# Kernel tuning notes

Measured on AMD Instinct MI355X. Metric: run time of the kernel, lower is better.

Reference implementation:

```python
import jax, jax.numpy as jnp
import numpy as np

B, S, D = 16, 1024, 768
H = 12
HD = D // H  # 64


def setup_inputs() -> dict:
    key = jax.random.key(0)
    k1, k2, k3 = jax.random.split(key, 3)
    scale_in = 1.0 / np.sqrt(D)
    return {
        "x": jax.random.normal(k1, (B, S, D), dtype=jnp.float32),
        "w_qkv": jax.random.normal(k2, (3 * D, D), dtype=jnp.float32) * scale_in,
        "b_qkv": jnp.zeros((3 * D,), dtype=jnp.float32),
        "w_proj": jax.random.normal(k3, (D, D), dtype=jnp.float32) * scale_in,
        "b_proj": jnp.zeros((D,), dtype=jnp.float32),
    }


def reference(x, w_qkv, b_qkv, w_proj, b_proj):
    b, s, d = x.shape
    scale = HD ** -0.5
    # qkv projection: [B,S,3D] -> [3,B,H,S,HD]
    qkv = x @ w_qkv.T + b_qkv
    qkv = qkv.reshape(b, s, 3, H, HD).transpose(2, 0, 3, 1, 4)
    q, k, v = qkv[0], qkv[1], qkv[2]
    q = q * scale
    attn = jnp.einsum("bhqd,bhkd->bhqk", q, k)  # [B,H,S,S]
    attn = jax.nn.softmax(attn, axis=-1)
    # attn_dropout is identity in eval mode
    z = jnp.einsum("bhqk,bhkd->bhqd", attn, v)
    z = z.transpose(0, 2, 1, 3).reshape(b, s, d)
    return z @ w_proj.T + b_proj
```

## Files before the change

### kernel.cpp

```cpp
#include <hip/hip_runtime.h>
#include <hip/hip_bf16.h>
#include <cstdint>
#include <cstddef>

typedef __attribute__((ext_vector_type(8))) short short8;
typedef __attribute__((ext_vector_type(4))) float floatx4;
typedef __attribute__((ext_vector_type(16))) float floatx16;
typedef unsigned short u16;

__device__ __forceinline__ u16 f2bf(float f) {
  unsigned u = __float_as_uint(f);
  u += 0x7FFFu + ((u >> 16) & 1u);
  return (u16)(u >> 16);
}

__device__ __forceinline__ unsigned cvt_pk_bf16(float a, float b) {
  unsigned r;
  asm("v_cvt_pk_bf16_f32 %0, %1, %2" : "=v"(r) : "v"(a), "v"(b));
  return r;
}

__device__ __forceinline__ float fexp2(float x) {
#if __has_builtin(__builtin_amdgcn_exp2f)
  return __builtin_amdgcn_exp2f(x);
#else
  float r;
  asm("v_exp_f32 %0, %1\n\ts_nop 1" : "=v"(r) : "v"(x));
  return r;
#endif
}

__device__ __forceinline__ float frcp(float x) {
#if __has_builtin(__builtin_amdgcn_rcpf)
  return __builtin_amdgcn_rcpf(x);
#else
  float r;
  asm("v_rcp_f32 %0, %1\n\ts_nop 1" : "=v"(r) : "v"(x));
  return r;
#endif
}

__device__ __forceinline__ void gload16(const u16* g, u16* l) {
  __builtin_amdgcn_global_load_lds(
      (const __attribute__((address_space(1))) void*)g,
      (__attribute__((address_space(3))) void*)l, 16, 0, 0);
}

__device__ __forceinline__ void phase_barrier() {
  __builtin_amdgcn_sched_barrier(0);
  __builtin_amdgcn_s_barrier();
  __builtin_amdgcn_sched_barrier(0);
}

#define MFMA16(a, b, c) __builtin_amdgcn_mfma_f32_16x16x32_bf16((a), (b), (c), 0, 0, 0)

__global__ void cvt3_kernel(const float* __restrict__ a, u16* __restrict__ oa, int na4,
                            const float* __restrict__ b, u16* __restrict__ ob, int nb4,
                            const float* __restrict__ c, u16* __restrict__ oc, int nc4) {
  int i = blockIdx.x * blockDim.x + threadIdx.x;
  int stride = gridDim.x * blockDim.x;
  int ntot = na4 + nb4 + nc4;
  for (int idx = i; idx < ntot; idx += stride) {
    const float* src; u16* dst; int j = idx;
    if (j < na4)            { src = a; dst = oa; }
    else if (j < na4 + nb4) { src = b; dst = ob; j -= na4; }
    else                    { src = c; dst = oc; j -= na4 + nb4; }
    float4 v = reinterpret_cast<const float4*>(src)[j];
    ushort4 o = make_ushort4(f2bf(v.x), f2bf(v.y), f2bf(v.z), f2bf(v.w));
    reinterpret_cast<ushort4*>(dst)[j] = o;
  }
}

template<bool OUTF32>
__global__ __launch_bounds__(512) void gemm_bt256_8p(
    const u16* __restrict__ A, const u16* __restrict__ B,
    const float* __restrict__ bias, void* __restrict__ Cout,
    int M, int N, int K, int qcols, float qscale)
{
  __shared__ u16 As[4 * 8192];
  __shared__ u16 Bs[4 * 8192];
  const int tid = threadIdx.x;
  const int lane = tid & 63, w = tid >> 6;
  const int l15 = lane & 15, lhi = lane >> 4;
  const int wm = w >> 2, wn = w & 3;

  const int mblocks = M >> 8;
  const int nb = N >> 8;
  const int bid = blockIdx.x;
  const int xcd = bid & 7;
  const int local = bid >> 3;
  const int mpx = mblocks >> 3;
  const int m0 = (xcd * mpx + local / nb) << 8;
  const int n0 = (local % nb) << 8;

  const int trow = tid >> 3;
  const int cg8 = ((tid & 7) ^ ((tid >> 4) & 7)) * 8;
  const u16* aS = A + (size_t)(m0 + trow) * K + cg8;
  const u16* bS = B + (size_t)(n0 + trow) * K + cg8;
  const int ksteps = K >> 6;

  const int x7 = (l15 >> 1) & 7;
  const int ko0 = l15 * 64 + (lhi ^ x7) * 8;
  const int ko1 = l15 * 64 + ((4 + lhi) ^ x7) * 8;
  const int brow = (wn & 1) * 64;

  floatx4 acc[8][4] = {};

#define STG(matS, lds, v, h) do { \
    gload16((matS) + (size_t)((h) * 128) * K + (size_t)(v) * 64, \
            (lds) + ((((v) & 1) * 2 + (h)) * 8192) + w * 512); \
    gload16((matS) + (size_t)((h) * 128 + 64) * K + (size_t)(v) * 64, \
            (lds) + ((((v) & 1) * 2 + (h)) * 8192) + 4096 + w * 512); \
  } while (0)

  STG(aS, As, 0, 0); STG(aS, As, 0, 1);
  STG(bS, Bs, 0, 0); STG(bS, Bs, 0, 1);
  if (ksteps > 1) {
    STG(bS, Bs, 1, 0); STG(bS, Bs, 1, 1);
    asm volatile("s_waitcnt vmcnt(4)" ::: "memory");
  } else {
    asm volatile("s_waitcnt vmcnt(0)" ::: "memory");
  }
  phase_barrier();

  for (int u = 0; u < ksteps; ++u) {
    const int so = (u & 1) * 16384;
    const u16* Ab = As + so + wm * 8192;
    const u16* Bb = Bs + so + (wn >> 1) * 8192;
    short8 af[4][2], bf[4][2];

#pragma unroll
    for (int i = 0; i < 4; ++i) {
      af[i][0] = *reinterpret_cast<const short8*>(Ab + (i * 16) * 64 + ko0);
      af[i][1] = *reinterpret_cast<const short8*>(Ab + (i * 16) * 64 + ko1);
    }
#pragma unroll
    for (int j = 0; j < 2; ++j) {
      bf[j][0] = *reinterpret_cast<const short8*>(Bb + (brow + j * 16) * 64 + ko0);
      bf[j][1] = *reinterpret_cast<const short8*>(Bb + (brow + j * 16) * 64 + ko1);
    }
    if (u + 1 < ksteps) STG(aS, As, u + 1, 0);
    phase_barrier();
    __builtin_amdgcn_s_setprio(1);
#pragma unroll
    for (int i = 0; i < 4; ++i)
#pragma unroll
      for (int j = 0; j < 2; ++j) {
        acc[i][j] = MFMA16(af[i][0], bf[j][0], acc[i][j]);
        acc[i][j] = MFMA16(af[i][1], bf[j][1], acc[i][j]);
      }
    __builtin_amdgcn_s_setprio(0);
    phase_barrier();

#pragma unroll
    for (int j = 2; j < 4; ++j) {
      bf[j][0] = *reinterpret_cast<const short8*>(Bb + (brow + 32 + (j - 2) * 16) * 64 + ko0);
      bf[j][1] = *reinterpret_cast<const short8*>(Bb + (brow + 32 + (j - 2) * 16) * 64 + ko1);
    }
    if (u + 1 < ksteps) STG(aS, As, u + 1, 1);
    phase_barrier();
    __builtin_amdgcn_s_setprio(1);
#pragma unroll
    for (int i = 0; i < 4; ++i)
#pragma unroll
      for (int j = 2; j < 4; ++j) {
        acc[i][j] = MFMA16(af[i][0], bf[j][0], acc[i][j]);
        acc[i][j] = MFMA16(af[i][1], bf[j][1], acc[i][j]);
      }
    __builtin_amdgcn_s_setprio(0);
    phase_barrier();

#pragma unroll
    for (int i = 0; i < 4; ++i) {
      af[i][0] = *reinterpret_cast<const short8*>(Ab + (64 + i * 16) * 64 + ko0);
      af[i][1] = *reinterpret_cast<const short8*>(Ab + (64 + i * 16) * 64 + ko1);
    }
    if (u + 2 < ksteps) STG(bS, Bs, u + 2, 0);
    phase_barrier();
    __builtin_amdgcn_s_setprio(1);
#pragma unroll
    for (int i = 0; i < 4; ++i)
#pragma unroll
      for (int j = 0; j < 2; ++j) {
        acc[4 + i][j] = MFMA16(af[i][0], bf[j][0], acc[4 + i][j]);
        acc[4 + i][j] = MFMA16(af[i][1], bf[j][1], acc[4 + i][j]);
      }
    __builtin_amdgcn_s_setprio(0);
    phase_barrier();

    if (u + 2 < ksteps) STG(bS, Bs, u + 2, 1);
    phase_barrier();
    __builtin_amdgcn_s_setprio(1);
#pragma unroll
    for (int i = 0; i < 4; ++i)
#pragma unroll
      for (int j = 2; j < 4; ++j) {
        acc[4 + i][j] = MFMA16(af[i][0], bf[j][0], acc[4 + i][j]);
        acc[4 + i][j] = MFMA16(af[i][1], bf[j][1], acc[4 + i][j]);
      }
    __builtin_amdgcn_s_setprio(0);
    if (u + 1 < ksteps) {
      if (u + 2 < ksteps) asm volatile("s_waitcnt vmcnt(4)" ::: "memory");
      else                asm volatile("s_waitcnt vmcnt(0)" ::: "memory");
    }
    phase_barrier();
  }
#undef STG

#pragma unroll
  for (int i = 0; i < 8; ++i)
#pragma unroll
    for (int j = 0; j < 4; ++j) {
      int row = m0 + wm * 128 + i * 16 + lhi * 4;
      int col = n0 + wn * 64 + j * 16 + l15;
      float bv = bias[col];
      float sc = (col < qcols) ? qscale : 1.0f;
#pragma unroll
      for (int r = 0; r < 4; ++r) {
        float v = (acc[i][j][r] + bv) * sc;
        if (OUTF32) reinterpret_cast<float*>(Cout)[(size_t)(row + r) * N + col] = v;
        else        reinterpret_cast<u16*>(Cout)[(size_t)(row + r) * N + col] = f2bf(v);
      }
    }
}

__global__ __launch_bounds__(256) void vtrans_kernel(
    const u16* __restrict__ qkv, u16* __restrict__ vt)
{
  __shared__ u16 T[64][72];
  const int idx = blockIdx.x;
  const int st = idx & 15;
  const int bh = idx >> 4;
  const int b = bh / 12, h = bh % 12;
  const int t = threadIdx.x;
  const int r2 = t >> 3, c8 = (t & 7) * 8;

  const u16* src = qkv + ((size_t)(b * 1024 + st * 64)) * 2304 + 1536 + h * 64;
#pragma unroll
  for (int rr = 0; rr < 2; ++rr) {
    int s = rr * 32 + r2;
    short8 v = *reinterpret_cast<const short8*>(src + (size_t)s * 2304 + c8);
    *reinterpret_cast<short8*>(&T[s][c8]) = v;
  }
  __syncthreads();
  u16* dst = vt + (size_t)bh * 64 * 1024 + st * 64;
#pragma unroll
  for (int rr = 0; rr < 2; ++rr) {
    int d = rr * 32 + r2;
    short8 o;
#pragma unroll
    for (int j = 0; j < 8; ++j) o[j] = T[c8 + j][d];
    *reinterpret_cast<short8*>(dst + (size_t)d * 1024 + c8) = o;
  }
}

__global__ __launch_bounds__(512) void attn9_kernel(
    const u16* __restrict__ qkv, const u16* __restrict__ vt, u16* __restrict__ z)
{
  constexpr int LDK = 72;
  constexpr int SLOT = 64 * LDK;
  __shared__ u16 Ks[2 * SLOT];
  __shared__ u16 Vs[2 * SLOT];

  const int tid = threadIdx.x;
  const int lane = tid & 63, w = tid >> 6;
  const int l31 = lane & 31, hi = lane >> 5;

  const int idx = blockIdx.x;
  const int head = idx % 192;
  const int qt   = idx / 192;
  const int b = head / 12, h = head % 12;

  const size_t rowbase = (size_t)b * 1024;
  const u16* Qp  = qkv + rowbase * 2304 + h * 64;
  const u16* Kp  = Qp + 768;
  const u16* Vtp = vt + (size_t)head * 64 * 1024;

  const int q0 = qt * 256 + w * 32;

  short8 qf[4];
#pragma unroll
  for (int c = 0; c < 4; ++c)
    qf[c] = *reinterpret_cast<const short8*>(
        Qp + (size_t)(q0 + l31) * 2304 + c * 16 + hi * 8);

  union { unsigned u[4]; short8 v; } ONE;
#pragma unroll
  for (int i = 0; i < 4; ++i) ONE.u[i] = 0x3F803F80u;
  const short8 ones = ONE.v;

  const int srow = tid >> 3, scol = (tid & 7) * 8;

  const u16* kstage = Kp + (size_t)srow * 2304 + scol;
  const u16* vstage = Vtp + (size_t)srow * 1024 + scol;
  constexpr size_t KADV = (size_t)64 * 2304;
  constexpr size_t VADV = 64;

  u16* const ksw = &Ks[srow * LDK + scol];
  u16* const vsw = &Vs[srow * LDK + scol];
  const u16* const ks0 = &Ks[l31 * LDK + hi * 8];
  const u16* const vs0 = &Vs[l31 * LDK + hi * 8];

  short8 kvr = *reinterpret_cast<const short8*>(kstage);
  short8 vvr = *reinterpret_cast<const short8*>(vstage);
  kstage += KADV; vstage += VADV;

  floatx16 oacc0 = {}, oacc1 = {}, lacc = {};

  for (int kt = 0; kt < 16; ++kt) {
    const int so = (kt & 1) * SLOT;
    *reinterpret_cast<short8*>(ksw + so) = kvr;
    *reinterpret_cast<short8*>(vsw + so) = vvr;
    __syncthreads();

    if (kt < 15) {
      kvr = *reinterpret_cast<const short8*>(kstage);
      vvr = *reinterpret_cast<const short8*>(vstage);
      kstage += KADV; vstage += VADV;
    }

    const u16* ka = ks0 + so;
    const u16* va = vs0 + so;

    floatx16 s0 = {}, s1 = {};
    __builtin_amdgcn_s_setprio(1);
#pragma unroll
    for (int c = 0; c < 4; ++c) {
      short8 kf0 = *reinterpret_cast<const short8*>(ka + c * 16);
      short8 kf1 = *reinterpret_cast<const short8*>(ka + 32 * LDK + c * 16);
      s0 = __builtin_amdgcn_mfma_f32_32x32x16_bf16(kf0, qf[c], s0, 0, 0, 0);
      s1 = __builtin_amdgcn_mfma_f32_32x32x16_bf16(kf1, qf[c], s1, 0, 0, 0);
    }
    __builtin_amdgcn_s_setprio(0);

#pragma unroll
    for (int r = 0; r < 16; ++r) {
      s0[r] = fexp2(s0[r]);
      s1[r] = fexp2(s1[r]);
    }

    short8 pa[4];
#pragma unroll
    for (int c = 0; c < 4; ++c) {
      const floatx16& sv = (c >> 1) ? s1 : s0;
      const int B0 = (c & 1) * 8, B1 = B0 + 4;
      unsigned x0 = cvt_pk_bf16(sv[B0],     sv[B0 + 1]);
      unsigned x1 = cvt_pk_bf16(sv[B0 + 2], sv[B0 + 3]);
      unsigned y0 = cvt_pk_bf16(sv[B1],     sv[B1 + 1]);
      unsigned y1 = cvt_pk_bf16(sv[B1 + 2], sv[B1 + 3]);
      asm("s_nop 1\n\tv_permlane32_swap_b32 %0, %1" : "+v"(x0), "+v"(y0));
      asm("s_nop 1\n\tv_permlane32_swap_b32 %0, %1" : "+v"(x1), "+v"(y1));
      union { unsigned u[4]; short8 v; } P;
      P.u[0] = x0; P.u[1] = x1; P.u[2] = y0; P.u[3] = y1;
      pa[c] = P.v;
    }

    __builtin_amdgcn_s_setprio(1);
#pragma unroll
    for (int c = 0; c < 4; ++c) {
      short8 vf0 = *reinterpret_cast<const short8*>(va + c * 16);
      short8 vf1 = *reinterpret_cast<const short8*>(va + 32 * LDK + c * 16);
      oacc0 = __builtin_amdgcn_mfma_f32_32x32x16_bf16(pa[c], vf0, oacc0, 0, 0, 0);
      oacc1 = __builtin_amdgcn_mfma_f32_32x32x16_bf16(pa[c], vf1, oacc1, 0, 0, 0);
      lacc  = __builtin_amdgcn_mfma_f32_32x32x16_bf16(pa[c], ones, lacc, 0, 0, 0);
    }
    __builtin_amdgcn_s_setprio(0);
  }

#pragma unroll
  for (int r = 0; r < 16; ++r) {
    int q = (r & 3) + 8 * (r >> 2) + 4 * hi;
    float li = frcp(lacc[r]);
    size_t orow = (rowbase + q0 + q) * (size_t)768 + h * 64;
    z[orow + l31]      = f2bf(oacc0[r] * li);
    z[orow + 32 + l31] = f2bf(oacc1[r] * li);
  }
}

extern "C" void kernel_launch(void* const* d_in, const int* in_sizes, int n_in,
                              void* d_out, int out_size, void* d_ws, size_t ws_size,
                              hipStream_t stream) {
  (void)in_sizes; (void)n_in; (void)out_size; (void)ws_size;
  const float* x      = (const float*)d_in[0];
  const float* w_qkv  = (const float*)d_in[1];
  const float* b_qkv  = (const float*)d_in[2];
  const float* w_proj = (const float*)d_in[3];
  const float* b_proj = (const float*)d_in[4];
  float* out = (float*)d_out;

  const int BS = 16 * 1024;
  const int D = 768, N3 = 2304;
  const float QSC = 0.180336880f;

  u16* xb  = (u16*)d_ws;
  u16* wqb = xb  + (size_t)BS * D;
  u16* wpb = wqb + (size_t)N3 * D;
  u16* qkv = wpb + (size_t)D * D;
  u16* zb  = qkv + (size_t)BS * N3;
  u16* vtb = xb;

  cvt3_kernel<<<2048, 256, 0, stream>>>(x, xb, BS * D / 4,
                                        w_qkv, wqb, N3 * D / 4,
                                        w_proj, wpb, D * D / 4);

  gemm_bt256_8p<false><<<(BS / 256) * (N3 / 256), 512, 0, stream>>>(
      xb, wqb, b_qkv, qkv, BS, N3, D, 768, QSC);
  vtrans_kernel<<<192 * 16, 256, 0, stream>>>(qkv, vtb);
  attn9_kernel<<<192 * 4, 512, 0, stream>>>(qkv, vtb, zb);
  gemm_bt256_8p<true><<<(BS / 256) * (D / 256), 512, 0, stream>>>(
      zb, wpb, b_proj, out, BS, D, D, 0, 1.0f);
}
```

Baseline: 208.9 us.

## Give each attention wave 64 queries and compute row sums with VALU

The attention kernel now runs with 256 threads and four waves. Each wave handles 64 query rows as two 32-row sub-tiles, so every K/V fragment read from LDS serves twice as much MFMA work. The softmax denominator, formerly an extra MFMA against a ones vector, is now a VALU sum of the exponentials plus a cross-half shuffle, and each row's sum is gathered with ds_bpermute in the epilogue. In exchange, register pressure per wave roughly doubles and there are fewer waves per block to hide latency.

```diff
diff --git a/kernel.cpp b/kernel.cpp
--- a/kernel.cpp
+++ b/kernel.cpp
@@ -254,7 +254,7 @@
   }
 }
 
-__global__ __launch_bounds__(512) void attn9_kernel(
+__global__ __launch_bounds__(256) void attn10_kernel(
     const u16* __restrict__ qkv, const u16* __restrict__ vt, u16* __restrict__ z)
 {
   constexpr int LDK = 72;
@@ -276,104 +276,128 @@
   const u16* Kp  = Qp + 768;
   const u16* Vtp = vt + (size_t)head * 64 * 1024;
 
-  const int q0 = qt * 256 + w * 32;
-
-  short8 qf[4];
-#pragma unroll
-  for (int c = 0; c < 4; ++c)
-    qf[c] = *reinterpret_cast<const short8*>(
-        Qp + (size_t)(q0 + l31) * 2304 + c * 16 + hi * 8);
-
-  union { unsigned u[4]; short8 v; } ONE;
-#pragma unroll
-  for (int i = 0; i < 4; ++i) ONE.u[i] = 0x3F803F80u;
-  const short8 ones = ONE.v;
-
-  const int srow = tid >> 3, scol = (tid & 7) * 8;
-
-  const u16* kstage = Kp + (size_t)srow * 2304 + scol;
-  const u16* vstage = Vtp + (size_t)srow * 1024 + scol;
+  const int q0 = qt * 256 + w * 64;
+
+  short8 qf[2][4];
+#pragma unroll
+  for (int s = 0; s < 2; ++s)
+#pragma unroll
+    for (int c = 0; c < 4; ++c)
+      qf[s][c] = *reinterpret_cast<const short8*>(
+          Qp + (size_t)(q0 + s * 32 + l31) * 2304 + c * 16 + hi * 8);
+
+  const int r0 = tid >> 3, c8 = (tid & 7) * 8;
+  const u16* kstage = Kp + (size_t)r0 * 2304 + c8;
+  const u16* vstage = Vtp + (size_t)r0 * 1024 + c8;
   constexpr size_t KADV = (size_t)64 * 2304;
   constexpr size_t VADV = 64;
 
-  u16* const ksw = &Ks[srow * LDK + scol];
-  u16* const vsw = &Vs[srow * LDK + scol];
+  u16* const ksw = &Ks[r0 * LDK + c8];
+  u16* const vsw = &Vs[r0 * LDK + c8];
   const u16* const ks0 = &Ks[l31 * LDK + hi * 8];
   const u16* const vs0 = &Vs[l31 * LDK + hi * 8];
 
-  short8 kvr = *reinterpret_cast<const short8*>(kstage);
-  short8 vvr = *reinterpret_cast<const short8*>(vstage);
+  short8 kvr0 = *reinterpret_cast<const short8*>(kstage);
+  short8 kvr1 = *reinterpret_cast<const short8*>(kstage + 32 * 2304);
+  short8 vvr0 = *reinterpret_cast<const short8*>(vstage);
+  short8 vvr1 = *reinterpret_cast<const short8*>(vstage + 32 * 1024);
   kstage += KADV; vstage += VADV;
 
-  floatx16 oacc0 = {}, oacc1 = {}, lacc = {};
+  floatx16 oacc[2][2] = {};
+  float lsum[2] = {0.f, 0.f};
 
   for (int kt = 0; kt < 16; ++kt) {
     const int so = (kt & 1) * SLOT;
-    *reinterpret_cast<short8*>(ksw + so) = kvr;
-    *reinterpret_cast<short8*>(vsw + so) = vvr;
+    *reinterpret_cast<short8*>(ksw + so)            = kvr0;
+    *reinterpret_cast<short8*>(ksw + so + 32 * LDK) = kvr1;
+    *reinterpret_cast<short8*>(vsw + so)            = vvr0;
+    *reinterpret_cast<short8*>(vsw + so + 32 * LDK) = vvr1;
     __syncthreads();
 
     if (kt < 15) {
-      kvr = *reinterpret_cast<const short8*>(kstage);
-      vvr = *reinterpret_cast<const short8*>(vstage);
+      kvr0 = *reinterpret_cast<const short8*>(kstage);
+      kvr1 = *reinterpret_cast<const short8*>(kstage + 32 * 2304);
+      vvr0 = *reinterpret_cast<const short8*>(vstage);
+      vvr1 = *reinterpret_cast<const short8*>(vstage + 32 * 1024);
       kstage += KADV; vstage += VADV;
     }
 
-    const u16* ka = ks0 + so;
-    const u16* va = vs0 + so;
-
-    floatx16 s0 = {}, s1 = {};
+    short8 kf[8];
+#pragma unroll
+    for (int c = 0; c < 4; ++c) {
+      kf[c]     = *reinterpret_cast<const short8*>(ks0 + so + c * 16);
+      kf[4 + c] = *reinterpret_cast<const short8*>(ks0 + so + 32 * LDK + c * 16);
+    }
+
+    short8 pa[2][4];
+#pragma unroll
+    for (int s = 0; s < 2; ++s) {
+      floatx16 s0 = {}, s1 = {};
+      __builtin_amdgcn_s_setprio(1);
+#pragma unroll
+      for (int c = 0; c < 4; ++c) {
+        s0 = __builtin_amdgcn_mfma_f32_32x32x16_bf16(kf[c],     qf[s][c], s0, 0, 0, 0);
+        s1 = __builtin_amdgcn_mfma_f32_32x32x16_bf16(kf[4 + c], qf[s][c], s1, 0, 0, 0);
+      }
+      __builtin_amdgcn_s_setprio(0);
+
+      float t0 = 0.f, t1 = 0.f, t2 = 0.f, t3 = 0.f;
+#pragma unroll
+      for (int r = 0; r < 16; r += 4) {
+        float e0 = fexp2(s0[r]),     e1 = fexp2(s0[r + 1]);
+        float e2 = fexp2(s0[r + 2]), e3 = fexp2(s0[r + 3]);
+        s0[r] = e0; s0[r + 1] = e1; s0[r + 2] = e2; s0[r + 3] = e3;
+        t0 += e0; t1 += e1; t2 += e2; t3 += e3;
+        float f0 = fexp2(s1[r]),     f1 = fexp2(s1[r + 1]);
+        float f2 = fexp2(s1[r + 2]), f3 = fexp2(s1[r + 3]);
+        s1[r] = f0; s1[r + 1] = f1; s1[r + 2] = f2; s1[r + 3] = f3;
+        t0 += f0; t1 += f1; t2 += f2; t3 += f3;
+      }
+      float ts = (t0 + t1) + (t2 + t3);
+      ts += __shfl_xor(ts, 32, 64);
+      lsum[s] += ts;
+
+#pragma unroll
+      for (int c = 0; c < 4; ++c) {
+        const floatx16& sv = (c >> 1) ? s1 : s0;
+        const int B0 = (c & 1) * 8, B1 = B0 + 4;
+        unsigned x0 = cvt_pk_bf16(sv[B0],     sv[B0 + 1]);
+        unsigned x1 = cvt_pk_bf16(sv[B0 + 2], sv[B0 + 3]);
+        unsigned y0 = cvt_pk_bf16(sv[B1],     sv[B1 + 1]);
+        unsigned y1 = cvt_pk_bf16(sv[B1 + 2], sv[B1 + 3]);
+        asm("s_nop 1\n\tv_permlane32_swap_b32 %0, %1" : "+v"(x0), "+v"(y0));
+        asm("s_nop 1\n\tv_permlane32_swap_b32 %0, %1" : "+v"(x1), "+v"(y1));
+        union { unsigned u[4]; short8 v; } P;
+        P.u[0] = x0; P.u[1] = x1; P.u[2] = y0; P.u[3] = y1;
+        pa[s][c] = P.v;
+      }
+    }
+
     __builtin_amdgcn_s_setprio(1);
 #pragma unroll
     for (int c = 0; c < 4; ++c) {
-      short8 kf0 = *reinterpret_cast<const short8*>(ka + c * 16);
-      short8 kf1 = *reinterpret_cast<const short8*>(ka + 32 * LDK + c * 16);
-      s0 = __builtin_amdgcn_mfma_f32_32x32x16_bf16(kf0, qf[c], s0, 0, 0, 0);
-      s1 = __builtin_amdgcn_mfma_f32_32x32x16_bf16(kf1, qf[c], s1, 0, 0, 0);
+      short8 vf0 = *reinterpret_cast<const short8*>(vs0 + so + c * 16);
+      short8 vf1 = *reinterpret_cast<const short8*>(vs0 + so + 32 * LDK + c * 16);
+      oacc[0][0] = __builtin_amdgcn_mfma_f32_32x32x16_bf16(pa[0][c], vf0, oacc[0][0], 0, 0, 0);
+      oacc[0][1] = __builtin_amdgcn_mfma_f32_32x32x16_bf16(pa[0][c], vf1, oacc[0][1], 0, 0, 0);
+      oacc[1][0] = __builtin_amdgcn_mfma_f32_32x32x16_bf16(pa[1][c], vf0, oacc[1][0], 0, 0, 0);
+      oacc[1][1] = __builtin_amdgcn_mfma_f32_32x32x16_bf16(pa[1][c], vf1, oacc[1][1], 0, 0, 0);
     }
     __builtin_amdgcn_s_setprio(0);
-
+  }
+
+#pragma unroll
+  for (int s = 0; s < 2; ++s) {
 #pragma unroll
     for (int r = 0; r < 16; ++r) {
-      s0[r] = fexp2(s0[r]);
-      s1[r] = fexp2(s1[r]);
-    }
-
-    short8 pa[4];
-#pragma unroll
-    for (int c = 0; c < 4; ++c) {
-      const floatx16& sv = (c >> 1) ? s1 : s0;
-      const int B0 = (c & 1) * 8, B1 = B0 + 4;
-      unsigned x0 = cvt_pk_bf16(sv[B0],     sv[B0 + 1]);
-      unsigned x1 = cvt_pk_bf16(sv[B0 + 2], sv[B0 + 3]);
-      unsigned y0 = cvt_pk_bf16(sv[B1],     sv[B1 + 1]);
-      unsigned y1 = cvt_pk_bf16(sv[B1 + 2], sv[B1 + 3]);
-      asm("s_nop 1\n\tv_permlane32_swap_b32 %0, %1" : "+v"(x0), "+v"(y0));
-      asm("s_nop 1\n\tv_permlane32_swap_b32 %0, %1" : "+v"(x1), "+v"(y1));
-      union { unsigned u[4]; short8 v; } P;
-      P.u[0] = x0; P.u[1] = x1; P.u[2] = y0; P.u[3] = y1;
-      pa[c] = P.v;
-    }
-
-    __builtin_amdgcn_s_setprio(1);
-#pragma unroll
-    for (int c = 0; c < 4; ++c) {
-      short8 vf0 = *reinterpret_cast<const short8*>(va + c * 16);
-      short8 vf1 = *reinterpret_cast<const short8*>(va + 32 * LDK + c * 16);
-      oacc0 = __builtin_amdgcn_mfma_f32_32x32x16_bf16(pa[c], vf0, oacc0, 0, 0, 0);
-      oacc1 = __builtin_amdgcn_mfma_f32_32x32x16_bf16(pa[c], vf1, oacc1, 0, 0, 0);
-      lacc  = __builtin_amdgcn_mfma_f32_32x32x16_bf16(pa[c], ones, lacc, 0, 0, 0);
-    }
-    __builtin_amdgcn_s_setprio(0);
-  }
-
-#pragma unroll
-  for (int r = 0; r < 16; ++r) {
-    int q = (r & 3) + 8 * (r >> 2) + 4 * hi;
-    float li = frcp(lacc[r]);
-    size_t orow = (rowbase + q0 + q) * (size_t)768 + h * 64;
-    z[orow + l31]      = f2bf(oacc0[r] * li);
-    z[orow + 32 + l31] = f2bf(oacc1[r] * li);
+      int q = (r & 3) + 8 * (r >> 2) + 4 * hi;
+      float lq = __uint_as_float(
+          __builtin_amdgcn_ds_bpermute(((lane & 32) + q) * 4, __float_as_uint(lsum[s])));
+      float li = frcp(lq);
+      size_t orow = (rowbase + q0 + s * 32 + q) * (size_t)768 + h * 64;
+      z[orow + l31]      = f2bf(oacc[s][0][r] * li);
+      z[orow + 32 + l31] = f2bf(oacc[s][1][r] * li);
+    }
   }
 }
 
@@ -406,7 +430,7 @@
   gemm_bt256_8p<false><<<(BS / 256) * (N3 / 256), 512, 0, stream>>>(
       xb, wqb, b_qkv, qkv, BS, N3, D, 768, QSC);
   vtrans_kernel<<<192 * 16, 256, 0, stream>>>(qkv, vtb);
-  attn9_kernel<<<192 * 4, 512, 0, stream>>>(qkv, vtb, zb);
+  attn10_kernel<<<192 * 4, 256, 0, stream>>>(qkv, vtb, zb);
   gemm_bt256_8p<true><<<(BS / 256) * (D / 256), 512, 0, stream>>>(
       zb, wpb, b_proj, out, BS, D, D, 0, 1.0f);
 }
```

Measured after the change: 225.9 us. 8.1% more time.
